# Optimization experiments

Hardware: AMD Instinct MI355X
Metric: run time of the kernel (lower is better)

## Reference

```python
import jax, jax.numpy as jnp
import numpy as np

B, S, HID = 2, 2048, 2048
NH, NKV, D = 16, 8, 128
N_REP = NH // NKV
EPS = 1e-6
THETA = 10000.0


def setup_inputs() -> dict:
    key = jax.random.key(0)
    ks = jax.random.split(key, 6)
    s = 0.02
    return {
        "hidden_states": jax.random.normal(ks[0], (B, S, HID), jnp.float32),
        "attention_mask": jnp.ones((B, S), jnp.float32),
        "wq": jax.random.normal(ks[1], (HID, NH * D), jnp.float32) * s,
        "wk": jax.random.normal(ks[2], (HID, NKV * D), jnp.float32) * s,
        "wv": jax.random.normal(ks[3], (HID, NKV * D), jnp.float32) * s,
        "wo": jax.random.normal(ks[4], (NH * D, HID), jnp.float32) * s,
        "q_norm_w": jnp.ones((D,), jnp.float32),
        "k_norm_w": jnp.ones((D,), jnp.float32),
    }


def _rms_norm(x, w, eps=EPS):
    # x: (..., D); computed in fp32 like the torch module
    x32 = x.astype(jnp.float32)
    var = jnp.mean(x32 * x32, axis=-1, keepdims=True)
    return (w * (x32 * jax.lax.rsqrt(var + eps))).astype(x.dtype)


def _rotate_half(x):
    x1, x2 = jnp.split(x, 2, axis=-1)
    return jnp.concatenate((-x2, x1), axis=-1)


def _rope_cos_sin(seq_len, dim, dtype):
    inv_freq = 1.0 / (THETA ** (jnp.arange(0, dim, 2, dtype=jnp.float32) / dim))
    t = jnp.arange(seq_len, dtype=jnp.float32)
    freqs = t[:, None] * inv_freq[None, :]          # (S, D/2)
    emb = jnp.concatenate((freqs, freqs), axis=-1)  # (S, D)
    # broadcast to (1, 1, S, D)
    return jnp.cos(emb).astype(dtype)[None, None], jnp.sin(emb).astype(dtype)[None, None]


def reference(hidden_states, attention_mask, wq, wk, wv, wo, q_norm_w, k_norm_w):
    b, s, _ = hidden_states.shape
    # QKV projections (bias-free)
    q = (hidden_states @ wq).reshape(b, s, NH, D).transpose(0, 2, 1, 3)   # (b, nh, s, d)
    k = (hidden_states @ wk).reshape(b, s, NKV, D).transpose(0, 2, 1, 3)  # (b, nkv, s, d)
    v = (hidden_states @ wv).reshape(b, s, NKV, D).transpose(0, 2, 1, 3)
    # per-head QK RMSNorm
    q = _rms_norm(q, q_norm_w)
    k = _rms_norm(k, k_norm_w)
    # RoPE
    cos, sin = _rope_cos_sin(s, D, q.dtype)
    q = q * cos + _rotate_half(q) * sin
    k = k * cos + _rotate_half(k) * sin
    # GQA repeat kv heads
    k = jnp.repeat(k, N_REP, axis=1)
    v = jnp.repeat(v, N_REP, axis=1)
    # SDPA (bidirectional, additive padding mask)
    scale = 1.0 / np.sqrt(D)
    scores = jnp.einsum("bhqd,bhkd->bhqk", q, k) * scale
    add_mask = (1.0 - attention_mask)[:, None, None, :] * jnp.finfo(scores.dtype).min
    scores = scores + add_mask
    attn = jax.nn.softmax(scores, axis=-1)
    out = jnp.einsum("bhqk,bhkd->bhqd", attn, v)
    out = out.transpose(0, 2, 1, 3).reshape(b, s, NH * D)
    return out @ wo
```

## Files before the change

kernel.cpp:

```cpp
#include <hip/hip_runtime.h>
#include <stdint.h>

#define BB   2
#define SS   2048
#define HID  2048
#define NHQ  16
#define NKV  8
#define DD   128
#define QKVW 4096

typedef __bf16 v8bf   __attribute__((ext_vector_type(8)));
typedef float  f32x4  __attribute__((ext_vector_type(4)));
typedef float  f32x16 __attribute__((ext_vector_type(16)));

__device__ __forceinline__ float bf2f(ushort u) {
    union { unsigned int i; float f; } x; x.i = ((unsigned int)u) << 16; return x.f;
}
__device__ __forceinline__ ushort f2bf(float f) {
    union { float f; unsigned int i; } x; x.f = f;
    unsigned int i = x.i;
    return (ushort)((i + 0x7fffu + ((i >> 16) & 1u)) >> 16);
}
__device__ __forceinline__ v8bf as_bf8(uint4 u) { return __builtin_bit_cast(v8bf, u); }

__device__ __forceinline__ unsigned int cvtpk_bf16(float lo, float hi) {
    unsigned int r;
    asm("v_cvt_pk_bf16_f32 %0, %1, %2" : "=v"(r) : "v"(lo), "v"(hi));
    return r;
}

__device__ __forceinline__ void store_el(float* p, float v)  { *p = v; }
__device__ __forceinline__ void store_el(ushort* p, float v) { *p = f2bf(v); }

__device__ __forceinline__ void gll16(const ushort* g, ushort* l) {
    __builtin_amdgcn_global_load_lds(
        (const __attribute__((address_space(1))) void*)g,
        (__attribute__((address_space(3))) void*)l, 16, 0, 0);
}

__device__ __forceinline__ int swz_off(int r, int lcolb) {
    return r * 64 + (((lcolb) ^ ((r & 4) << 3)) >> 1);
}
__device__ __forceinline__ int hswz(int r, int colb) {
    return r * 32 + (((colb) ^ ((r & 8) << 2)) >> 1);
}

#define PREP_CAST   8192
#define PREP_WQ     (PREP_CAST)
#define PREP_WK     (PREP_WQ + 4096)
#define PREP_WV     (PREP_WK + 2048)
#define PREP_WO     (PREP_WV + 2048)
#define PREP_ROPE   (PREP_WO + 4096)
#define PREP_TOTAL  (PREP_ROPE + 512)

__device__ __forceinline__ void tcast_body(
    const float* __restrict__ in, ushort* __restrict__ out,
    int K, int N, int bx, int by, int t)
{
    __shared__ float tile[32][33];
    int n0 = bx * 32, k0 = by * 32;
    int tx = t & 31, ty = t >> 5;
#pragma unroll
    for (int i = 0; i < 32; i += 8)
        tile[ty + i][tx] = in[(size_t)(k0 + ty + i) * N + n0 + tx];
    __syncthreads();
#pragma unroll
    for (int i = 0; i < 32; i += 8)
        out[(size_t)(n0 + ty + i) * K + k0 + tx] = f2bf(tile[tx][ty + i]);
}

__global__ __launch_bounds__(256) void prep(
    const float* __restrict__ X,  const float* __restrict__ wq,
    const float* __restrict__ wk, const float* __restrict__ wv,
    const float* __restrict__ wo,
    ushort* __restrict__ Xb, ushort* __restrict__ WqkvT, ushort* __restrict__ Wot,
    float2* __restrict__ rtab)
{
    int bid = blockIdx.x, t = threadIdx.x;
    if (bid < PREP_CAST) {
        int i = (bid * 256 + t) * 4;
        float4 v = *(const float4*)&X[i];
        ushort4 o = { f2bf(v.x), f2bf(v.y), f2bf(v.z), f2bf(v.w) };
        *(ushort4*)&Xb[i] = o;
    } else if (bid < PREP_WK) {
        int l = bid - PREP_WQ;
        tcast_body(wq, WqkvT, 2048, 2048, l & 63, l >> 6, t);
    } else if (bid < PREP_WV) {
        int l = bid - PREP_WK;
        tcast_body(wk, WqkvT + (size_t)2048 * 2048, 2048, 1024, l & 31, l >> 5, t);
    } else if (bid < PREP_WO) {
        int l = bid - PREP_WV;
        tcast_body(wv, WqkvT + (size_t)3072 * 2048, 2048, 1024, l & 31, l >> 5, t);
    } else if (bid < PREP_ROPE) {
        int l = bid - PREP_WO;
        tcast_body(wo, Wot, 2048, 2048, l & 63, l >> 6, t);
    } else {
        int e = (bid - PREP_ROPE) * 256 + t;
        int s = e >> 6, dp = e & 63;
        float inv = expf(-(float)dp * (1.0f / 64.0f) * 9.210340371976184f);
        float sn, cs;
        sincosf((float)s * inv, &sn, &cs);
        rtab[e] = make_float2(cs, sn);
    }
}

__global__ __launch_bounds__(512, 1) void gemm256(
    const ushort* __restrict__ A, const ushort* __restrict__ Bt,
    ushort* __restrict__ C, int M, int N, int K,
    const float* __restrict__ qnw, const float* __restrict__ knw,
    const float2* __restrict__ rtab)
{
    __shared__ __align__(16) ushort As[2][2][256 * 32];
    __shared__ __align__(16) ushort Bs[2][2][256 * 32];
    const int t = threadIdx.x;
    const int lane = t & 63, wave = t >> 6;
    const int quad = lane >> 4, l15 = lane & 15;
    const int m0 = blockIdx.y * 256, n0 = blockIdx.x * 256;
    const int wm = (wave >> 1) * 64;
    const int wn = (wave & 1) * 128;

    const f32x4 zv = {0.f, 0.f, 0.f, 0.f};
    f32x4 acc[4][8];
#pragma unroll
    for (int i = 0; i < 4; i++)
#pragma unroll
        for (int j = 0; j < 8; j++) acc[i][j] = zv;

    int srow[2], scol[2];
#pragma unroll
    for (int j = 0; j < 2; j++) {
        int p16 = (j * 512 + t) * 16;
        int lg = p16 ^ (((p16 >> 9) & 1) << 5);
        srow[j] = lg >> 6; scol[j] = (lg & 63) >> 1;
    }
    int aoff[4], boff[8];
#pragma unroll
    for (int mf = 0; mf < 4; mf++) aoff[mf] = hswz(wm + mf * 16 + l15, quad * 16);
#pragma unroll
    for (int nf = 0; nf < 8; nf++) boff[nf] = hswz(wn + nf * 16 + l15, quad * 16);

#define STAGE_HALF(buf, hh, kb)                                                          \
    {                                                                                    \
        _Pragma("unroll")                                                                \
        for (int j = 0; j < 2; j++)                                                      \
            gll16(&A[(size_t)(m0 + srow[j]) * K + (kb) + scol[j]],                       \
                  &As[buf][hh][(j * 512 + t) * 8]);                                      \
        _Pragma("unroll")                                                                \
        for (int j = 0; j < 2; j++)                                                      \
            gll16(&Bt[(size_t)(n0 + srow[j]) * K + (kb) + scol[j]],                      \
                  &Bs[buf][hh][(j * 512 + t) * 8]);                                      \
    }

    const int NT = K >> 6;

    STAGE_HALF(0, 0, 0);
    STAGE_HALF(0, 1, 32);
    asm volatile("s_waitcnt vmcnt(4)" ::: "memory");
    __builtin_amdgcn_s_barrier();

    uint4 af[4], bf[4];
    for (int T = 0; T < NT; T++) {
        const int c = T & 1;
        const bool stg = (T + 1) < NT;
        const int kn = (T + 1) << 6;

#pragma unroll
        for (int mf = 0; mf < 4; mf++) af[mf] = *(const uint4*)&As[c][0][aoff[mf]];
#pragma unroll
        for (int nf = 0; nf < 4; nf++) bf[nf] = *(const uint4*)&Bs[c][0][boff[nf]];
        if (stg) STAGE_HALF(c ^ 1, 0, kn);
        __builtin_amdgcn_s_barrier();
        asm volatile("s_waitcnt lgkmcnt(0)" ::: "memory");
        __builtin_amdgcn_sched_barrier(0);
        __builtin_amdgcn_s_setprio(1);
#pragma unroll
        for (int mf = 0; mf < 4; mf++)
#pragma unroll
            for (int nf = 0; nf < 4; nf++)
                acc[mf][nf] = __builtin_amdgcn_mfma_f32_16x16x32_bf16(
                    as_bf8(af[mf]), as_bf8(bf[nf]), acc[mf][nf], 0, 0, 0);
        __builtin_amdgcn_s_setprio(0);
        __builtin_amdgcn_s_barrier();

#pragma unroll
        for (int nf = 0; nf < 4; nf++) bf[nf] = *(const uint4*)&Bs[c][0][boff[4 + nf]];
        __builtin_amdgcn_s_barrier();
        asm volatile("s_waitcnt lgkmcnt(0)" ::: "memory");
        __builtin_amdgcn_sched_barrier(0);
        __builtin_amdgcn_s_setprio(1);
#pragma unroll
        for (int mf = 0; mf < 4; mf++)
#pragma unroll
            for (int nf = 0; nf < 4; nf++)
                acc[mf][4 + nf] = __builtin_amdgcn_mfma_f32_16x16x32_bf16(
                    as_bf8(af[mf]), as_bf8(bf[nf]), acc[mf][4 + nf], 0, 0, 0);
        __builtin_amdgcn_s_setprio(0);
        if (stg) asm volatile("s_waitcnt vmcnt(4)" ::: "memory");
        else     asm volatile("s_waitcnt vmcnt(0)" ::: "memory");
        __builtin_amdgcn_s_barrier();

#pragma unroll
        for (int mf = 0; mf < 4; mf++) af[mf] = *(const uint4*)&As[c][1][aoff[mf]];
#pragma unroll
        for (int nf = 0; nf < 4; nf++) bf[nf] = *(const uint4*)&Bs[c][1][boff[nf]];
        if (stg) STAGE_HALF(c ^ 1, 1, kn + 32);
        __builtin_amdgcn_s_barrier();
        asm volatile("s_waitcnt lgkmcnt(0)" ::: "memory");
        __builtin_amdgcn_sched_barrier(0);
        __builtin_amdgcn_s_setprio(1);
#pragma unroll
        for (int mf = 0; mf < 4; mf++)
#pragma unroll
            for (int nf = 0; nf < 4; nf++)
                acc[mf][nf] = __builtin_amdgcn_mfma_f32_16x16x32_bf16(
                    as_bf8(af[mf]), as_bf8(bf[nf]), acc[mf][nf], 0, 0, 0);
        __builtin_amdgcn_s_setprio(0);
        __builtin_amdgcn_s_barrier();

#pragma unroll
        for (int nf = 0; nf < 4; nf++) bf[nf] = *(const uint4*)&Bs[c][1][boff[4 + nf]];
        __builtin_amdgcn_s_barrier();
        asm volatile("s_waitcnt lgkmcnt(0)" ::: "memory");
        __builtin_amdgcn_sched_barrier(0);
        __builtin_amdgcn_s_setprio(1);
#pragma unroll
        for (int mf = 0; mf < 4; mf++)
#pragma unroll
            for (int nf = 0; nf < 4; nf++)
                acc[mf][4 + nf] = __builtin_amdgcn_mfma_f32_16x16x32_bf16(
                    as_bf8(af[mf]), as_bf8(bf[nf]), acc[mf][4 + nf], 0, 0, 0);
        __builtin_amdgcn_s_setprio(0);
        if (stg) {
            asm volatile("s_waitcnt vmcnt(4)" ::: "memory");
            __builtin_amdgcn_s_barrier();
        }
    }
#undef STAGE_HALF

    const int col0 = n0 + wn;
    if (col0 >= 3072) {
#pragma unroll
        for (int mf = 0; mf < 4; mf++)
#pragma unroll
            for (int nf = 0; nf < 8; nf++)
#pragma unroll
                for (int r = 0; r < 4; r++) {
                    int row = m0 + wm + mf * 16 + quad * 4 + r;
                    C[(size_t)row * N + col0 + nf * 16 + l15] = f2bf(acc[mf][nf][r]);
                }
    } else {
        const bool isq = col0 < 2048;
        const float* nw = isq ? qnw : knw;
        const float scl = isq ? (0.08838834764831845f * 1.4426950408889634f) : 1.0f;
        float wgt[8];
#pragma unroll
        for (int nf = 0; nf < 8; nf++) wgt[nf] = nw[nf * 16 + l15];
#pragma unroll
        for (int mf = 0; mf < 4; mf++)
#pragma unroll
            for (int r = 0; r < 4; r++) {
                int row = m0 + wm + mf * 16 + quad * 4 + r;
                float v[8];
#pragma unroll
                for (int nf = 0; nf < 8; nf++) v[nf] = acc[mf][nf][r];
                float sum = 0.f;
#pragma unroll
                for (int nf = 0; nf < 8; nf++) sum = fmaf(v[nf], v[nf], sum);
#pragma unroll
                for (int xm = 1; xm < 16; xm <<= 1) sum += __shfl_xor(sum, xm, 64);
                float rr = rsqrtf(sum * (1.0f / 128.0f) + 1e-6f);
                int s = row & (SS - 1);
#pragma unroll
                for (int nf0 = 0; nf0 < 4; nf0++) {
                    float2 cs = rtab[s * 64 + nf0 * 16 + l15];
                    float x = v[nf0] * rr * wgt[nf0];
                    float y = v[nf0 + 4] * rr * wgt[nf0 + 4];
                    C[(size_t)row * N + col0 + nf0 * 16 + l15] =
                        f2bf((x * cs.x - y * cs.y) * scl);
                    C[(size_t)row * N + col0 + 64 + nf0 * 16 + l15] =
                        f2bf((y * cs.x + x * cs.y) * scl);
                }
            }
    }
}

template <typename OutT>
__global__ __launch_bounds__(512, 2) void gemm_bt2(
    const ushort* __restrict__ A, const ushort* __restrict__ Bt,
    OutT* __restrict__ C, int M, int N, int K)
{
    __shared__ __align__(16) ushort As[3][256 * 64];
    __shared__ __align__(16) ushort Bs[3][128 * 64];
    const int t = threadIdx.x;
    const int lane = t & 63, wave = t >> 6;
    const int quad = lane >> 4, l15 = lane & 15;
    const int m0 = blockIdx.y * 256, n0 = blockIdx.x * 128;
    const int wm = (wave >> 1) * 64;
    const int wn = (wave & 1) * 64;

    const f32x4 zv = {0.f, 0.f, 0.f, 0.f};
    f32x4 acc[4][4];
#pragma unroll
    for (int i = 0; i < 4; i++)
#pragma unroll
        for (int j = 0; j < 4; j++) acc[i][j] = zv;

    int arow[4], acol[4];
#pragma unroll
    for (int j = 0; j < 4; j++) {
        int p = (j * 512 + t) * 16;
        int l = p ^ (((p >> 9) & 1) << 5);
        arow[j] = l >> 7; acol[j] = (l & 127) >> 1;
    }
    int brow[2], bcol[2];
#pragma unroll
    for (int j = 0; j < 2; j++) {
        int p = (j * 512 + t) * 16;
        int l = p ^ (((p >> 9) & 1) << 5);
        brow[j] = l >> 7; bcol[j] = (l & 127) >> 1;
    }

    int aoff[4][2], boff[2][2][2];
#pragma unroll
    for (int mf = 0; mf < 4; mf++)
#pragma unroll
        for (int kk = 0; kk < 2; kk++)
            aoff[mf][kk] = swz_off(wm + mf * 16 + l15, kk * 64 + quad * 16);
#pragma unroll
    for (int q = 0; q < 2; q++)
#pragma unroll
        for (int nf = 0; nf < 2; nf++)
#pragma unroll
            for (int kk = 0; kk < 2; kk++)
                boff[q][nf][kk] = swz_off(wn + q * 32 + nf * 16 + l15, kk * 64 + quad * 16);

#define STAGE_A(j, slot, kk0) \
    gll16(&A[(size_t)(m0 + arow[j]) * K + (kk0) + acol[j]], &As[slot][0] + ((j) * 512 + t) * 8)
#define STAGE_B(j, slot, kk0) \
    gll16(&Bt[(size_t)(n0 + brow[j]) * K + (kk0) + bcol[j]], &Bs[slot][0] + ((j) * 512 + t) * 8)

    const int NT = K >> 6;

#pragma unroll
    for (int j = 0; j < 4; j++) STAGE_A(j, 0, 0);
#pragma unroll
    for (int j = 0; j < 2; j++) STAGE_B(j, 0, 0);
#pragma unroll
    for (int j = 0; j < 4; j++) STAGE_A(j, 1, 64);
#pragma unroll
    for (int j = 0; j < 2; j++) STAGE_B(j, 1, 64);
    asm volatile("s_waitcnt vmcnt(6)" ::: "memory");
    __builtin_amdgcn_s_barrier();

    int cur = 0;
    for (int T = 0; T < NT; T++) {
        const ushort* Ac = &As[cur][0];
        const ushort* Bc = &Bs[cur][0];
        int stg = cur + 2; if (stg >= 3) stg -= 3;
        const int k2 = (T + 2) << 6;
        const bool do_stage = (T + 2) < NT;

        uint4 af[4][2], bf[2][2];
#pragma unroll
        for (int mf = 0; mf < 4; mf++)
#pragma unroll
            for (int kk = 0; kk < 2; kk++)
                af[mf][kk] = *(const uint4*)&Ac[aoff[mf][kk]];
#pragma unroll
        for (int nf = 0; nf < 2; nf++)
#pragma unroll
            for (int kk = 0; kk < 2; kk++)
                bf[nf][kk] = *(const uint4*)&Bc[boff[0][nf][kk]];
        if (do_stage) {
            STAGE_A(0, stg, k2); STAGE_A(1, stg, k2); STAGE_B(0, stg, k2);
        }
        __builtin_amdgcn_s_barrier();
        asm volatile("s_waitcnt lgkmcnt(0)" ::: "memory");
        __builtin_amdgcn_sched_barrier(0);
        __builtin_amdgcn_s_setprio(1);
#pragma unroll
        for (int mf = 0; mf < 4; mf++)
#pragma unroll
            for (int nf = 0; nf < 2; nf++)
#pragma unroll
                for (int kk = 0; kk < 2; kk++)
                    acc[mf][nf] = __builtin_amdgcn_mfma_f32_16x16x32_bf16(
                        as_bf8(af[mf][kk]), as_bf8(bf[nf][kk]), acc[mf][nf], 0, 0, 0);
        __builtin_amdgcn_s_setprio(0);
        __builtin_amdgcn_s_barrier();

#pragma unroll
        for (int nf = 0; nf < 2; nf++)
#pragma unroll
            for (int kk = 0; kk < 2; kk++)
                bf[nf][kk] = *(const uint4*)&Bc[boff[1][nf][kk]];
        if (do_stage) {
            STAGE_A(2, stg, k2); STAGE_A(3, stg, k2); STAGE_B(1, stg, k2);
            asm volatile("s_waitcnt vmcnt(6)" ::: "memory");
        } else if (T + 2 == NT) {
            asm volatile("s_waitcnt vmcnt(0)" ::: "memory");
        }
        __builtin_amdgcn_s_barrier();
        asm volatile("s_waitcnt lgkmcnt(0)" ::: "memory");
        __builtin_amdgcn_sched_barrier(0);
        __builtin_amdgcn_s_setprio(1);
#pragma unroll
        for (int mf = 0; mf < 4; mf++)
#pragma unroll
            for (int nf = 0; nf < 2; nf++)
#pragma unroll
                for (int kk = 0; kk < 2; kk++)
                    acc[mf][2 + nf] = __builtin_amdgcn_mfma_f32_16x16x32_bf16(
                        as_bf8(af[mf][kk]), as_bf8(bf[nf][kk]), acc[mf][2 + nf], 0, 0, 0);
        __builtin_amdgcn_s_setprio(0);
        __builtin_amdgcn_s_barrier();

        cur++; if (cur == 3) cur = 0;
    }
#undef STAGE_A
#undef STAGE_B

#pragma unroll
    for (int mf = 0; mf < 4; mf++)
#pragma unroll
        for (int nf = 0; nf < 4; nf++)
#pragma unroll
            for (int r = 0; r < 4; r++) {
                int row = m0 + wm + mf * 16 + quad * 4 + r;
                int col = n0 + wn + nf * 16 + l15;
                store_el(&C[(size_t)row * N + col], acc[mf][nf][r]);
            }
}

__global__ __launch_bounds__(256, 2) void flash_attn(
    const ushort* __restrict__ qkv, const float* __restrict__ mask, ushort* __restrict__ O)
{
    __shared__ __align__(16) ushort Ks[2][64 * 128];
    __shared__ __align__(16) ushort Vt[128 * 64];
    __shared__ __align__(16) float  Madd[SS];
    const int t = threadIdx.x;
    const int lane = t & 63, wave = t >> 6;
    const int l31 = lane & 31, half = lane >> 5;
    const int b = blockIdx.z, h = blockIdx.y, q0 = blockIdx.x * 128;
    const int kh = h >> 1;

#pragma unroll
    for (int i = 0; i < 2; i++) {
        int idx = i * 1024 + t * 4;
        float4 mv = *(const float4*)&mask[b * SS + idx];
        float4 o = { (1.f - mv.x) * -1e30f, (1.f - mv.y) * -1e30f,
                     (1.f - mv.z) * -1e30f, (1.f - mv.w) * -1e30f };
        *(float4*)&Madd[idx] = o;
    }

    uint4 aq[8];
    {
        const ushort* qp = qkv + ((size_t)(b * SS + q0 + wave * 32 + l31)) * QKVW + h * 128 + half * 8;
#pragma unroll
        for (int kt = 0; kt < 8; kt++) aq[kt] = *(const uint4*)&qp[kt * 16];
    }
    f32x16 acc_o[4];
#pragma unroll
    for (int i = 0; i < 4; i++)
#pragma unroll
        for (int r = 0; r < 16; r++) acc_o[i][r] = 0.f;
    float lp[4] = {0.f, 0.f, 0.f, 0.f};

    const ushort* Kg = qkv + (size_t)b * SS * QKVW + 2048 + kh * 128;
    const ushort* Vg = qkv + (size_t)b * SS * QKVW + 3072 + kh * 128;

    const int vp = t & 31, vdc = t >> 5;
    uint4 vreg[4];
#define LOAD_V(K0)                                                                  \
    {                                                                               \
        _Pragma("unroll")                                                           \
        for (int pass = 0; pass < 2; pass++) {                                      \
            int d0 = (vdc + pass * 8) * 8;                                          \
            vreg[pass * 2 + 0] = *(const uint4*)&Vg[(size_t)((K0) + 2 * vp) * QKVW + d0];     \
            vreg[pass * 2 + 1] = *(const uint4*)&Vg[(size_t)((K0) + 2 * vp + 1) * QKVW + d0]; \
        }                                                                           \
    }
#define STAGE_K(K0, buf)                                                            \
    {                                                                               \
        _Pragma("unroll")                                                           \
        for (int i = 0; i < 4; i++) {                                               \
            int chunk = i * 256 + t;                                                \
            int row = chunk >> 4, cp = chunk & 15;                                  \
            int cl = cp ^ (row & 15);                                               \
            gll16(&Kg[(size_t)((K0) + row) * QKVW + cl * 8], &Ks[buf][chunk * 8]);  \
        }                                                                           \
    }

    STAGE_K(0, 0);
    LOAD_V(0);

    for (int k0 = 0; k0 < SS; k0 += 64) {
        const int cur = (k0 >> 6) & 1;
        __syncthreads();
        if (k0 + 64 < SS) STAGE_K(k0 + 64, cur ^ 1);
#pragma unroll
        for (int pass = 0; pass < 2; pass++) {
            const ushort* pa_ = (const ushort*)&vreg[pass * 2 + 0];
            const ushort* pb_ = (const ushort*)&vreg[pass * 2 + 1];
            int d0 = (vdc + pass * 8) * 8;
#pragma unroll
            for (int j = 0; j < 8; j++) {
                int cp = (vp >> 2) ^ j;
                unsigned int v = (unsigned int)pa_[j] | ((unsigned int)pb_[j] << 16);
                *(unsigned int*)&Vt[(d0 + j) * 64 + cp * 8 + (vp & 3) * 2] = v;
            }
        }
        if (k0 + 64 < SS) LOAD_V(k0 + 64);
        asm volatile("s_waitcnt lgkmcnt(0)" ::: "memory");
        __builtin_amdgcn_sched_barrier(0);
        __builtin_amdgcn_s_barrier();

        f32x16 sc[2];
#pragma unroll
        for (int nt = 0; nt < 2; nt++)
#pragma unroll
            for (int g = 0; g < 4; g++) {
                f32x4 em = *(const f32x4*)&Madd[k0 + nt * 32 + 4 * half + g * 8];
#pragma unroll
                for (int j = 0; j < 4; j++) sc[nt][g * 4 + j] = em[j];
            }
        __builtin_amdgcn_s_setprio(1);
#pragma unroll
        for (int nt = 0; nt < 2; nt++) {
#pragma unroll
            for (int kt = 0; kt < 8; kt++) {
                int cp = (kt * 2 + half) ^ (l31 & 15);
                uint4 bk = *(const uint4*)&Ks[cur][(nt * 32 + l31) * 128 + cp * 8];
                sc[nt] = __builtin_amdgcn_mfma_f32_32x32x16_bf16(
                    as_bf8(bk), as_bf8(aq[kt]), sc[nt], 0, 0, 0);
            }
        }
        __builtin_amdgcn_s_setprio(0);

        uint4 pa[4];
#pragma unroll
        for (int nt = 0; nt < 2; nt++) {
            float p[16];
#pragma unroll
            for (int r = 0; r < 16; r++) {
                float pv = __builtin_amdgcn_exp2f(sc[nt][r]);
                p[r] = pv;
                lp[r & 3] += pv;
            }
            unsigned int pk[8];
#pragma unroll
            for (int i = 0; i < 8; i++) pk[i] = cvtpk_bf16(p[2 * i], p[2 * i + 1]);
            auto sA = __builtin_amdgcn_permlane32_swap(pk[0], pk[2], false, false);
            auto sB = __builtin_amdgcn_permlane32_swap(pk[1], pk[3], false, false);
            auto sC = __builtin_amdgcn_permlane32_swap(pk[4], pk[6], false, false);
            auto sD = __builtin_amdgcn_permlane32_swap(pk[5], pk[7], false, false);
            uint4 f0, f1;
            f0.x = sA[0]; f0.y = sB[0]; f0.z = sA[1]; f0.w = sB[1];
            f1.x = sC[0]; f1.y = sD[0]; f1.z = sC[1]; f1.w = sD[1];
            pa[nt * 2 + 0] = f0;
            pa[nt * 2 + 1] = f1;
        }

        __builtin_amdgcn_s_setprio(1);
#pragma unroll
        for (int kt2 = 0; kt2 < 4; kt2++) {
            int kc = kt2 * 2 + half;
            int co = (kc ^ (l31 & 7)) * 8;
#pragma unroll
            for (int nt = 0; nt < 4; nt++) {
                uint4 bv = *(const uint4*)&Vt[(nt * 32 + l31) * 64 + co];
                acc_o[nt] = __builtin_amdgcn_mfma_f32_32x32x16_bf16(
                    as_bf8(pa[kt2]), as_bf8(bv), acc_o[nt], 0, 0, 0);
            }
        }
        __builtin_amdgcn_s_setprio(0);
    }
    float lsum = (lp[0] + lp[1]) + (lp[2] + lp[3]);
    lsum += __shfl_xor(lsum, 32, 64);
    float linv = 1.0f / lsum;
    float li[16];
#pragma unroll
    for (int r = 0; r < 16; r++)
        li[r] = __shfl(linv, (r & 3) + 8 * (r >> 2) + 4 * half, 64);
#pragma unroll
    for (int nt = 0; nt < 4; nt++)
#pragma unroll
        for (int r = 0; r < 16; r++) {
            int prow = (r & 3) + 8 * (r >> 2) + 4 * half;
            int qrow = q0 + wave * 32 + prow;
            int d = nt * 32 + l31;
            float v = acc_o[nt][r] * li[r];
            O[((size_t)(b * SS + qrow)) * (NHQ * DD) + h * 128 + d] = f2bf(v);
        }
}

extern "C" void kernel_launch(void* const* d_in, const int* in_sizes, int n_in,
                              void* d_out, int out_size, void* d_ws, size_t ws_size,
                              hipStream_t stream)
{
    const float* X    = (const float*)d_in[0];
    const float* mask = (const float*)d_in[1];
    const float* wq   = (const float*)d_in[2];
    const float* wk   = (const float*)d_in[3];
    const float* wv   = (const float*)d_in[4];
    const float* wo   = (const float*)d_in[5];
    const float* qnw  = (const float*)d_in[6];
    const float* knw  = (const float*)d_in[7];
    float* out = (float*)d_out;

    const size_t M = (size_t)BB * SS;
    ushort* Xb    = (ushort*)d_ws;
    ushort* WqkvT = Xb    + M * HID;
    ushort* Wot   = WqkvT + (size_t)4096 * HID;
    ushort* QKV   = Wot   + (size_t)2048 * 2048;
    ushort* Obuf  = QKV   + M * QKVW;
    float2* rtab  = (float2*)(Obuf + M * (size_t)(NHQ * DD));

    prep<<<PREP_TOTAL, 256, 0, stream>>>(X, wq, wk, wv, wo, Xb, WqkvT, Wot, rtab);

    gemm256<<<dim3(4096 / 256, 4096 / 256), 512, 0, stream>>>(
        Xb, WqkvT, QKV, 4096, 4096, 2048, qnw, knw, rtab);

    flash_attn<<<dim3(SS / 128, NHQ, BB), 256, 0, stream>>>(QKV, mask, Obuf);

    gemm_bt2<float><<<dim3(2048 / 128, 4096 / 256), 512, 0, stream>>>(Obuf, Wot, out, 4096, 2048, 2048);
}
```

Before: 333.1 us.

## Switch QKV GEMM to a three-slot K=32 ring buffer with prefetch distance two

Replaces the double-buffered pair of K=32 halves with a three-slot ring of K=32 tiles. Each iteration loads the tile for T+2 while computing T, splitting the A and B loads across the two MFMA halves. The goal is to keep loads further ahead of compute and drop some barriers, while using less LDS (three slots instead of four). The trade-off is more loop iterations and more dependence on vmcnt and barrier ordering being correct.

```diff
diff --git a/kernel.cpp b/kernel.cpp
--- a/kernel.cpp
+++ b/kernel.cpp
@@ -104,14 +104,14 @@
     }
 }
 
-__global__ __launch_bounds__(512, 1) void gemm256(
+__global__ __launch_bounds__(512, 1) void gemm_qkv(
     const ushort* __restrict__ A, const ushort* __restrict__ Bt,
     ushort* __restrict__ C, int M, int N, int K,
     const float* __restrict__ qnw, const float* __restrict__ knw,
     const float2* __restrict__ rtab)
 {
-    __shared__ __align__(16) ushort As[2][2][256 * 32];
-    __shared__ __align__(16) ushort Bs[2][2][256 * 32];
+    __shared__ __align__(16) ushort As[3][256 * 32];
+    __shared__ __align__(16) ushort Bs[3][256 * 32];
     const int t = threadIdx.x;
     const int lane = t & 63, wave = t >> 6;
     const int quad = lane >> 4, l15 = lane & 15;
@@ -139,36 +139,42 @@
 #pragma unroll
     for (int nf = 0; nf < 8; nf++) boff[nf] = hswz(wn + nf * 16 + l15, quad * 16);
 
-#define STAGE_HALF(buf, hh, kb)                                                          \
-    {                                                                                    \
-        _Pragma("unroll")                                                                \
-        for (int j = 0; j < 2; j++)                                                      \
-            gll16(&A[(size_t)(m0 + srow[j]) * K + (kb) + scol[j]],                       \
-                  &As[buf][hh][(j * 512 + t) * 8]);                                      \
-        _Pragma("unroll")                                                                \
-        for (int j = 0; j < 2; j++)                                                      \
-            gll16(&Bt[(size_t)(n0 + srow[j]) * K + (kb) + scol[j]],                      \
-                  &Bs[buf][hh][(j * 512 + t) * 8]);                                      \
-    }
-
-    const int NT = K >> 6;
-
-    STAGE_HALF(0, 0, 0);
-    STAGE_HALF(0, 1, 32);
+#define STAGE_AQ(slot, kb)                                                           \
+    {                                                                                \
+        _Pragma("unroll")                                                            \
+        for (int j = 0; j < 2; j++)                                                  \
+            gll16(&A[(size_t)(m0 + srow[j]) * K + (kb) + scol[j]],                   \
+                  &As[slot][(j * 512 + t) * 8]);                                     \
+    }
+#define STAGE_BQ(slot, kb)                                                           \
+    {                                                                                \
+        _Pragma("unroll")                                                            \
+        for (int j = 0; j < 2; j++)                                                  \
+            gll16(&Bt[(size_t)(n0 + srow[j]) * K + (kb) + scol[j]],                  \
+                  &Bs[slot][(j * 512 + t) * 8]);                                     \
+    }
+
+    const int NT = K >> 5;
+
+    STAGE_AQ(0, 0); STAGE_BQ(0, 0);
+    STAGE_AQ(1, 32); STAGE_BQ(1, 32);
     asm volatile("s_waitcnt vmcnt(4)" ::: "memory");
     __builtin_amdgcn_s_barrier();
 
-    uint4 af[4], bf[4];
+    int cur = 0;
     for (int T = 0; T < NT; T++) {
-        const int c = T & 1;
-        const bool stg = (T + 1) < NT;
-        const int kn = (T + 1) << 6;
-
-#pragma unroll
-        for (int mf = 0; mf < 4; mf++) af[mf] = *(const uint4*)&As[c][0][aoff[mf]];
-#pragma unroll
-        for (int nf = 0; nf < 4; nf++) bf[nf] = *(const uint4*)&Bs[c][0][boff[nf]];
-        if (stg) STAGE_HALF(c ^ 1, 0, kn);
+        const ushort* Ac = &As[cur][0];
+        const ushort* Bc = &Bs[cur][0];
+        int stg = cur + 2; if (stg >= 3) stg -= 3;
+        const int k2 = (T + 2) << 5;
+        const bool do_stage = (T + 2) < NT;
+
+        uint4 af[4], bf[4];
+#pragma unroll
+        for (int mf = 0; mf < 4; mf++) af[mf] = *(const uint4*)&Ac[aoff[mf]];
+#pragma unroll
+        for (int nf = 0; nf < 4; nf++) bf[nf] = *(const uint4*)&Bc[boff[nf]];
+        if (do_stage) STAGE_AQ(stg, k2);
         __builtin_amdgcn_s_barrier();
         asm volatile("s_waitcnt lgkmcnt(0)" ::: "memory");
         __builtin_amdgcn_sched_barrier(0);
@@ -183,7 +189,13 @@
         __builtin_amdgcn_s_barrier();
 
 #pragma unroll
-        for (int nf = 0; nf < 4; nf++) bf[nf] = *(const uint4*)&Bs[c][0][boff[4 + nf]];
+        for (int nf = 0; nf < 4; nf++) bf[nf] = *(const uint4*)&Bc[boff[4 + nf]];
+        if (do_stage) {
+            STAGE_BQ(stg, k2);
+            asm volatile("s_waitcnt vmcnt(4)" ::: "memory");
+        } else if (T + 2 == NT) {
+            asm volatile("s_waitcnt vmcnt(0)" ::: "memory");
+        }
         __builtin_amdgcn_s_barrier();
         asm volatile("s_waitcnt lgkmcnt(0)" ::: "memory");
         __builtin_amdgcn_sched_barrier(0);
@@ -195,47 +207,12 @@
                 acc[mf][4 + nf] = __builtin_amdgcn_mfma_f32_16x16x32_bf16(
                     as_bf8(af[mf]), as_bf8(bf[nf]), acc[mf][4 + nf], 0, 0, 0);
         __builtin_amdgcn_s_setprio(0);
-        if (stg) asm volatile("s_waitcnt vmcnt(4)" ::: "memory");
-        else     asm volatile("s_waitcnt vmcnt(0)" ::: "memory");
-        __builtin_amdgcn_s_barrier();
-
-#pragma unroll
-        for (int mf = 0; mf < 4; mf++) af[mf] = *(const uint4*)&As[c][1][aoff[mf]];
-#pragma unroll
-        for (int nf = 0; nf < 4; nf++) bf[nf] = *(const uint4*)&Bs[c][1][boff[nf]];
-        if (stg) STAGE_HALF(c ^ 1, 1, kn + 32);
-        __builtin_amdgcn_s_barrier();
-        asm volatile("s_waitcnt lgkmcnt(0)" ::: "memory");
-        __builtin_amdgcn_sched_barrier(0);
-        __builtin_amdgcn_s_setprio(1);
-#pragma unroll
-        for (int mf = 0; mf < 4; mf++)
-#pragma unroll
-            for (int nf = 0; nf < 4; nf++)
-                acc[mf][nf] = __builtin_amdgcn_mfma_f32_16x16x32_bf16(
-                    as_bf8(af[mf]), as_bf8(bf[nf]), acc[mf][nf], 0, 0, 0);
-        __builtin_amdgcn_s_setprio(0);
-        __builtin_amdgcn_s_barrier();
-
-#pragma unroll
-        for (int nf = 0; nf < 4; nf++) bf[nf] = *(const uint4*)&Bs[c][1][boff[4 + nf]];
-        __builtin_amdgcn_s_barrier();
-        asm volatile("s_waitcnt lgkmcnt(0)" ::: "memory");
-        __builtin_amdgcn_sched_barrier(0);
-        __builtin_amdgcn_s_setprio(1);
-#pragma unroll
-        for (int mf = 0; mf < 4; mf++)
-#pragma unroll
-            for (int nf = 0; nf < 4; nf++)
-                acc[mf][4 + nf] = __builtin_amdgcn_mfma_f32_16x16x32_bf16(
-                    as_bf8(af[mf]), as_bf8(bf[nf]), acc[mf][4 + nf], 0, 0, 0);
-        __builtin_amdgcn_s_setprio(0);
-        if (stg) {
-            asm volatile("s_waitcnt vmcnt(4)" ::: "memory");
-            __builtin_amdgcn_s_barrier();
-        }
-    }
-#undef STAGE_HALF
+        __builtin_amdgcn_s_barrier();
+
+        cur++; if (cur == 3) cur = 0;
+    }
+#undef STAGE_AQ
+#undef STAGE_BQ
 
     const int col0 = n0 + wn;
     if (col0 >= 3072) {
@@ -618,7 +595,7 @@
 
     prep<<<PREP_TOTAL, 256, 0, stream>>>(X, wq, wk, wv, wo, Xb, WqkvT, Wot, rtab);
 
-    gemm256<<<dim3(4096 / 256, 4096 / 256), 512, 0, stream>>>(
+    gemm_qkv<<<dim3(4096 / 256, 4096 / 256), 512, 0, stream>>>(
         Xb, WqkvT, QKV, 4096, 4096, 2048, qnw, knw, rtab);
 
     flash_attn<<<dim3(SS / 128, NHQ, BB), 256, 0, stream>>>(QKV, mask, Obuf);
```

New measurement: 326.8 us (median of 3 runs). Within noise of the previous version (-1.9%).
